# Optimization experiments

Hardware: AMD Instinct MI355X
Metric: run time of the kernel (lower is better)

## Reference

```python
import jax, jax.numpy as jnp
import numpy as np

B, S, D, F = 32, 512, 1024, 4096
R_COMMON, R_DOMAIN, E = 16, 16, 8
ALPHA = 2.0


def setup_inputs() -> dict:
    key = jax.random.key(0)
    ks = jax.random.split(key, 12)
    sd = lambda k, shape: jax.random.normal(k, shape, dtype=jnp.float32) * (1.0 / np.sqrt(shape[-1]))
    return {
        "hidden_states": jax.random.normal(ks[0], (B, S, D), dtype=jnp.float32),
        "expert_ids": jax.random.randint(ks[1], (B,), 0, E, dtype=jnp.int32),
        # nn.Linear weights: [out_features, in_features]
        "wi": sd(ks[2], (F, D)),
        "wo": sd(ks[3], (D, F)),
        "common_wi_a": sd(ks[4], (R_COMMON, D)),
        "common_wi_b": sd(ks[5], (F, R_COMMON)),
        "common_wo_a": sd(ks[6], (R_COMMON, F)),
        "common_wo_b": sd(ks[7], (D, R_COMMON)),
        # stacked per-expert LoRA weights
        "experts_wi_a": sd(ks[8], (E, R_DOMAIN, D)),
        "experts_wi_b": sd(ks[9], (F, R_DOMAIN)) * jnp.ones((E, 1, 1)) * 0.0 + sd(ks[9], (E, F, R_DOMAIN)),
        "experts_wo_a": sd(ks[10], (E, R_DOMAIN, F)),
        "experts_wo_b": sd(ks[11], (E, D, R_DOMAIN)),
    }


def _expert_lora(x, expert_ids, Wa, Wb):
    """Per-row (dim 0) expert LoRA correction, vectorized via gather.

    x: [B, S, din]; Wa: [E, r, din]; Wb: [E, dout, r].
    Equivalent to the per-expert mask-gather/scatter-add loop since each
    row belongs to exactly one expert.
    """
    Ab = Wa[expert_ids]  # [B, r, din]
    Bb = Wb[expert_ids]  # [B, dout, r]
    low = jnp.einsum("bsd,brd->bsr", x, Ab)
    return ALPHA * jnp.einsum("bsr,bor->bso", low, Bb)


def reference(hidden_states, expert_ids, wi, wo,
              common_wi_a, common_wi_b, common_wo_a, common_wo_b,
              experts_wi_a, experts_wi_b, experts_wo_a, experts_wo_b):
    x = hidden_states
    hidden_i = jnp.einsum("bsd,fd->bsf", x, wi)
    hidden_i += ALPHA * jnp.einsum("bsr,fr->bsf", jnp.einsum("bsd,rd->bsr", x, common_wi_a), common_wi_b)
    hidden_i += _expert_lora(x, expert_ids, experts_wi_a, experts_wi_b)
    hidden_i = jax.nn.relu(hidden_i)  # dense_act_fn='relu'; dropout is identity (eval)
    hidden_o = jnp.einsum("bsf,df->bsd", hidden_i, wo)
    hidden_o += ALPHA * jnp.einsum("bsr,dr->bsd", jnp.einsum("bsf,rf->bsr", hidden_i, common_wo_a), common_wo_b)
    hidden_o += _expert_lora(hidden_i, expert_ids, experts_wo_a, experts_wo_b)
    return hidden_o
```

## Files before the change

kernel.cpp:

```cpp
#include <hip/hip_runtime.h>
#include <hip/hip_bf16.h>
#include <stdint.h>

#define B_ 32
#define S_ 512
#define D_ 1024
#define F_ 4096
#define N_ (B_*S_)
#define E_ 8
#define ALPHA_ 2.0f

#define LDA1 1088
#define LDA2 4160

typedef __hip_bfloat16 bf16;
typedef __attribute__((ext_vector_type(8))) short short8;
typedef __attribute__((ext_vector_type(8))) __bf16 bf16x8;
typedef __attribute__((ext_vector_type(4))) float f32x4;

__device__ __forceinline__ f32x4 mfma_bf16(short8 a, short8 b, f32x4 c) {
    return __builtin_amdgcn_mfma_f32_16x16x32_bf16(
        __builtin_bit_cast(bf16x8, a), __builtin_bit_cast(bf16x8, b), c, 0, 0, 0);
}

__device__ __forceinline__ void gload_lds16(const void* g, void* l) {
    __builtin_amdgcn_global_load_lds((const __attribute__((address_space(1))) void*)g,
                                     (__attribute__((address_space(3))) void*)l, 16, 0, 0);
}

__device__ __forceinline__ unsigned pack2(float a, float b) {
    unsigned short x = __builtin_bit_cast(unsigned short, __float2bfloat16(a));
    unsigned short y = __builtin_bit_cast(unsigned short, __float2bfloat16(b));
    return (unsigned)x | ((unsigned)y << 16);
}
__device__ __forceinline__ uint2 pack4(float4 v) {
    return make_uint2(pack2(v.x, v.y), pack2(v.z, v.w));
}

__global__ __launch_bounds__(256) void prep_w_kernel(
    const float* __restrict__ wi, const float* __restrict__ wo,
    const float* __restrict__ cwia, const float* __restrict__ cwib,
    const float* __restrict__ cwoa, const float* __restrict__ cwob,
    const float* __restrict__ ewia, const float* __restrict__ ewib,
    const float* __restrict__ ewoa, const float* __restrict__ ewob,
    bf16* __restrict__ wi_b, bf16* __restrict__ wo_b,
    bf16* __restrict__ ex1, bf16* __restrict__ ex2,
    bf16* __restrict__ wilo, bf16* __restrict__ wolo)
{
    const int tid0 = blockIdx.x * blockDim.x + threadIdx.x;
    const int stride = gridDim.x * blockDim.x;

    for (int i = tid0; i < F_*D_/4; i += stride) {
        ((uint2*)wi_b)[i] = pack4(((const float4*)wi)[i]);
        ((uint2*)wo_b)[i] = pack4(((const float4*)wo)[i]);
    }
    for (int i = tid0; i < E_*F_*16; i += stride) {
        int e = i >> 16; int rem = i & 0xFFFF; int f = rem >> 4; int r = rem & 15;
        bf16* dst = ex1 + (((size_t)e*F_ + f) << 6);
        dst[r]      = __float2bfloat16(cwib[f*16 + r]);
        dst[16 + r] = __float2bfloat16(ewib[(((size_t)e*F_ + f) << 4) + r]);
        dst[32 + r] = __float2bfloat16(0.f);
        dst[48 + r] = __float2bfloat16(0.f);
    }
    for (int i = tid0; i < E_*D_*16; i += stride) {
        int e = i >> 14; int rem = i & 0x3FFF; int d = rem >> 4; int r = rem & 15;
        bf16* dst = ex2 + (((size_t)e*D_ + d) << 6);
        dst[r]      = __float2bfloat16(cwob[d*16 + r]);
        dst[16 + r] = __float2bfloat16(ewob[(((size_t)e*D_ + d) << 4) + r]);
        dst[32 + r] = __float2bfloat16(0.f);
        dst[48 + r] = __float2bfloat16(0.f);
    }
    for (int i = tid0; i < E_*32*(D_/4); i += stride) {
        int e = i / (32*(D_/4)); int rem = i - e*(32*(D_/4));
        int r = rem / (D_/4); int c4 = (rem % (D_/4)) * 4;
        const float* src = (r < 16) ? (cwia + (size_t)r*D_ + c4)
                                    : (ewia + ((size_t)(e*16 + (r-16)))*D_ + c4);
        *(uint2*)(wilo + ((size_t)(e*32 + r))*D_ + c4) = pack4(*(const float4*)src);
    }
    for (int i = tid0; i < E_*32*(F_/4); i += stride) {
        int e = i / (32*(F_/4)); int rem = i - e*(32*(F_/4));
        int r = rem / (F_/4); int c4 = (rem % (F_/4)) * 4;
        const float* src = (r < 16) ? (cwoa + (size_t)r*F_ + c4)
                                    : (ewoa + ((size_t)(e*16 + (r-16)))*F_ + c4);
        *(uint2*)(wolo + ((size_t)(e*32 + r))*F_ + c4) = pack4(*(const float4*)src);
    }
}

__global__ __launch_bounds__(256) void prep_x_kernel(
    const float* __restrict__ x, bf16* __restrict__ A1)
{
    const int tid0 = blockIdx.x * blockDim.x + threadIdx.x;
    const int stride = gridDim.x * blockDim.x;
    for (int i = tid0; i < N_*(D_/4); i += stride) {
        int row = i >> 8; int c4 = (i & 255) << 2;
        float4 v = *(const float4*)(x + (size_t)i * 4);
        *(uint2*)(A1 + (size_t)row*LDA1 + c4) = pack4(v);
    }
    for (int i = tid0; i < N_*8; i += stride) {
        int row = i >> 3; int c = (i & 7) << 2;
        *(uint2*)(A1 + (size_t)row*LDA1 + 1056 + c) = make_uint2(0u, 0u);
    }
}

template<int K>
__global__ __launch_bounds__(256) void lowproj_kernel(
    const bf16* __restrict__ A, const bf16* __restrict__ W,
    const int* __restrict__ eids, bf16* __restrict__ Out,
    int lda, int kout)
{
    constexpr int BM = 64, BK = 64;
    __shared__ __align__(16) bf16 Asm[BM*BK];
    __shared__ __align__(16) bf16 Wsm[32*BK];

    const int tid = threadIdx.x;
    const int row0 = blockIdx.x * BM;
    const int e = eids[row0 >> 9];
    const int w = tid >> 6, lane = tid & 63;
    const int tr = tid >> 3, ts = tid & 7;
    const int lrow = lane & 15;
    const int lk16 = (lane >> 4) << 4;

    f32x4 acc[2] = {};

    int aoff, woff[2];
    { int r = w*16 + lrow; aoff = r*128 + (lk16 ^ ((r & 7) << 4)); }
    #pragma unroll
    for (int n = 0; n < 2; ++n) {
        int r = n*16 + lrow; woff[n] = r*128 + (lk16 ^ ((r & 7) << 4));
    }
    const bf16* Wp = W + (size_t)e * 32 * K;

    #pragma unroll 1
    for (int kt = 0; kt < K/BK; ++kt) {
        const int k0 = kt * BK;
        #pragma unroll
        for (int i = 0; i < 2; ++i) {
            int row = tr + 32*i;
            int slot = ts ^ (row & 7);
            gload_lds16(A + (size_t)(row0 + row)*lda + k0 + slot*8,
                        (char*)Asm + row*128 + ts*16);
        }
        {
            int row = tr;
            int slot = ts ^ (row & 7);
            gload_lds16(Wp + (size_t)row*K + k0 + slot*8,
                        (char*)Wsm + row*128 + ts*16);
        }
        __syncthreads();
        #pragma unroll
        for (int kk = 0; kk < 2; ++kk) {
            short8 a = *(const short8*)((const char*)Asm + (aoff ^ (kk << 6)));
            #pragma unroll
            for (int n = 0; n < 2; ++n) {
                short8 b = *(const short8*)((const char*)Wsm + (woff[n] ^ (kk << 6)));
                acc[n] = mfma_bf16(a, b, acc[n]);
            }
        }
        __syncthreads();
    }

    const int jrow = (lane >> 4) << 2;
    #pragma unroll
    for (int n = 0; n < 2; ++n) {
        #pragma unroll
        for (int j = 0; j < 4; ++j) {
            int r = row0 + w*16 + jrow + j;
            int c = n*16 + lrow;
            Out[(size_t)r*lda + kout + c] = __float2bfloat16(ALPHA_ * acc[n][j]);
        }
    }
    #pragma unroll
    for (int i = 0; i < 8; ++i) {
        int idx = tid*8 + i;
        int r = idx >> 5, c = idx & 31;
        Out[(size_t)(row0 + r)*lda + kout + 32 + c] = __float2bfloat16(0.f);
    }
}

#define DSREAD(base, off) (*(const short8*)((const char*)(base) + (off)))
#define VMW4 asm volatile("s_waitcnt vmcnt(4)" ::: "memory")
#define VMW2 asm volatile("s_waitcnt vmcnt(2)" ::: "memory")
#define VMW0 asm volatile("s_waitcnt vmcnt(0)" ::: "memory")
#define VMNONE (void)0
#define BAR __builtin_amdgcn_s_barrier()

#define STAGE_A_HALF(KTN, AL, h)                                           \
  { const bf16* gpA_ = Ag + (size_t)(KTN)*64;                              \
    int rA_ = tr + 64*(h);                                                 \
    int sA_ = ts ^ (rA_ & 7);                                              \
    gload_lds16(gpA_ + (size_t)rA_*LDAe + sA_*8,                           \
                (char*)(AL) + rA_*128 + ts*16);                            \
    int rA2_ = rA_ + 128;                                                  \
    gload_lds16(gpA_ + (size_t)rA2_*LDAe + sA_*8,                          \
                (char*)(AL) + rA2_*128 + ts*16); }

#define STAGE_B_HALF(KTN, BL, h)                                           \
  { const bf16* gpB_; int bldB_; int bkB_;                                 \
    if ((KTN) < KMAIN_EL/64) { gpB_ = Bg; bldB_ = LDBe; bkB_ = (KTN)*64; } \
    else                     { gpB_ = Bxg; bldB_ = 64; bkB_ = 0; }         \
    int rB_ = (tr & 31) + 64*(tr >> 5) + 32*(h);                           \
    int sB_ = ts ^ (rB_ & 7);                                              \
    gload_lds16(gpB_ + (size_t)rB_*bldB_ + bkB_ + sB_*8,                   \
                (char*)(BL) + rB_*128 + ts*16);                            \
    int rB2_ = rB_ + 128;                                                  \
    gload_lds16(gpB_ + (size_t)rB2_*bldB_ + bkB_ + sB_*8,                  \
                (char*)(BL) + rB2_*128 + ts*16); }

#define RD_AF(dst, AC, base)                                               \
  _Pragma("unroll") for (int m_ = 0; m_ < 4; ++m_)                         \
    _Pragma("unroll") for (int k_ = 0; k_ < 2; ++k_)                       \
      dst[m_][k_] = DSREAD(AC, aoff[(base)+m_] ^ (k_ << 6));

#define RD_BQ(dst, BC, base)                                               \
  _Pragma("unroll") for (int n_ = 0; n_ < 2; ++n_)                         \
    _Pragma("unroll") for (int k_ = 0; k_ < 2; ++k_)                       \
      dst[n_][k_] = DSREAD(BC, boff[(base)+n_] ^ (k_ << 6));

#define MFMA16(afr, bqr, mb, nb)                                           \
  __builtin_amdgcn_s_setprio(1);                                           \
  _Pragma("unroll") for (int m_ = 0; m_ < 4; ++m_)                         \
    _Pragma("unroll") for (int n_ = 0; n_ < 2; ++n_)                       \
      _Pragma("unroll") for (int k_ = 0; k_ < 2; ++k_)                     \
        acc[(mb)+m_][(nb)+n_] =                                            \
            mfma_bf16(afr[m_][k_], bqr[n_][k_], acc[(mb)+m_][(nb)+n_]);    \
  __builtin_amdgcn_s_setprio(0);

#define TILE8(AC, BC, DOSTAGE, AN, BN, KTN, W1, W2, W4)                    \
  {                                                                        \
    short8 afl[4][2], afh[4][2], bql[2][2], bqh[2][2];                     \
                         \
    RD_AF(afl, AC, 0); RD_BQ(bql, BC, 0);                                  \
    if (DOSTAGE) { STAGE_A_HALF(KTN, AN, 0); }                             \
    W1; BAR;                                                               \
    MFMA16(afl, bql, 0, 0);                                                \
                                                                  \
    RD_BQ(bqh, BC, 2);                                                     \
    if (DOSTAGE) { STAGE_B_HALF(KTN, BN, 0); }                             \
    W2; BAR;                                                               \
    MFMA16(afl, bqh, 0, 2);                                                \
                                                              \
    RD_AF(afh, AC, 4);                                                     \
    if (DOSTAGE) { STAGE_B_HALF(KTN, BN, 1); }                             \
    MFMA16(afh, bql, 4, 0);                                                \
    if (DOSTAGE) { STAGE_A_HALF(KTN, AN, 1); }                             \
    W4; BAR;                                                               \
    MFMA16(afh, bqh, 4, 2);                                                \
  }

template<int KMAIN_EL, int LDAe, int LDBe, int LDCe, int NCOLSe, bool RELU_BF16>
__global__ __launch_bounds__(512, 2) void gemm256_kernel(
    const bf16* __restrict__ A, const bf16* __restrict__ Bmain,
    const bf16* __restrict__ Bextra, const int* __restrict__ eids,
    void* __restrict__ C)
{
    constexpr int MT = N_/256;
    constexpr int NT = NCOLSe/256;
    constexpr int NWG = MT*NT;
    constexpr int KTILES = KMAIN_EL/64 + 1;
    static_assert((KTILES & 1) == 1, "pair loop + tail assumes odd KTILES");
    static_assert(NWG % 8 == 0, "xcd swizzle needs nwg%8==0");
    constexpr int CPX = NWG/8;

    __shared__ __align__(16) bf16 As[2][256*64];
    __shared__ __align__(16) bf16 Bs[2][256*64];

    const int bid = blockIdx.x;
    const int wg = (bid & 7) * CPX + (bid >> 3);
    const int mt = wg % MT, nt = wg / MT;
    const int arow0 = mt * 256, bcol0 = nt * 256;
    const int e = eids[arow0 >> 9];

    const int tid = threadIdx.x;
    const int lane = tid & 63;
    const int wid = tid >> 6;
    const int wm = wid >> 2, wn = wid & 3;
    const int tr = tid >> 3, ts = tid & 7;

    const bf16* Ag  = A + (size_t)arow0 * LDAe;
    const bf16* Bg  = Bmain + (size_t)bcol0 * LDBe;
    const bf16* Bxg = Bextra + ((size_t)e * NCOLSe + bcol0) * 64;

    int aoff[8], boff[4];
    const int lk16 = (lane >> 4) << 4;
    #pragma unroll
    for (int m = 0; m < 8; ++m) {
        int r = wm*128 + m*16 + (lane & 15);
        aoff[m] = r*128 + (lk16 ^ ((r & 7) << 4));
    }
    #pragma unroll
    for (int n = 0; n < 4; ++n) {
        int r = wn*64 + n*16 + (lane & 15);
        boff[n] = r*128 + (lk16 ^ ((r & 7) << 4));
    }

    f32x4 acc[8][4] = {};

    STAGE_A_HALF(0, As[0], 0);
    STAGE_B_HALF(0, Bs[0], 0);
    STAGE_B_HALF(0, Bs[0], 1);
    STAGE_A_HALF(0, As[0], 1);
    VMW4; BAR;

    #pragma unroll 1
    for (int t = 0; t < KTILES - 1; t += 2) {
        TILE8(As[0], Bs[0], true, As[1], Bs[1], t + 1, VMW4, VMW4, VMW4);
        TILE8(As[1], Bs[1], true, As[0], Bs[0], t + 2, VMW4, VMW4, VMW4);
    }
    TILE8(As[0], Bs[0], false, As[1], Bs[1], 0, VMW2, VMW0, VMNONE);

    const int jrow = (lane >> 4) << 2;
    if constexpr (RELU_BF16) {
        bf16* Cb = (bf16*)C;
        #pragma unroll
        for (int m = 0; m < 8; ++m)
            #pragma unroll
            for (int j = 0; j < 4; ++j) {
                size_t rbase = (size_t)(arow0 + wm*128 + m*16 + jrow + j) * LDCe;
                #pragma unroll
                for (int n = 0; n < 4; ++n) {
                    float v = acc[m][n][j];
                    v = v > 0.f ? v : 0.f;
                    Cb[rbase + bcol0 + wn*64 + n*16 + (lane & 15)] = __float2bfloat16(v);
                }
            }
    } else {
        float* Cf = (float*)C;
        #pragma unroll
        for (int m = 0; m < 8; ++m)
            #pragma unroll
            for (int j = 0; j < 4; ++j) {
                size_t rbase = (size_t)(arow0 + wm*128 + m*16 + jrow + j) * LDCe;
                #pragma unroll
                for (int n = 0; n < 4; ++n)
                    Cf[rbase + bcol0 + wn*64 + n*16 + (lane & 15)] = acc[m][n][j];
            }
    }
}

extern "C" void kernel_launch(void* const* d_in, const int* in_sizes, int n_in,
                              void* d_out, int out_size, void* d_ws, size_t ws_size,
                              hipStream_t stream)
{
    const float* x    = (const float*)d_in[0];
    const int*   eids = (const int*)d_in[1];
    const float* wi   = (const float*)d_in[2];
    const float* wo   = (const float*)d_in[3];
    const float* cwia = (const float*)d_in[4];
    const float* cwib = (const float*)d_in[5];
    const float* cwoa = (const float*)d_in[6];
    const float* cwob = (const float*)d_in[7];
    const float* ewia = (const float*)d_in[8];
    const float* ewib = (const float*)d_in[9];
    const float* ewoa = (const float*)d_in[10];
    const float* ewob = (const float*)d_in[11];

    char* p = (char*)d_ws;
    bf16* A1   = (bf16*)p; p += (size_t)N_*LDA1*sizeof(bf16);
    bf16* A2   = (bf16*)p; p += (size_t)N_*LDA2*sizeof(bf16);
    bf16* wi_b = (bf16*)p; p += (size_t)F_*D_*sizeof(bf16);
    bf16* wo_b = (bf16*)p; p += (size_t)D_*F_*sizeof(bf16);
    bf16* ex1  = (bf16*)p; p += (size_t)E_*F_*64*sizeof(bf16);
    bf16* ex2  = (bf16*)p; p += (size_t)E_*D_*64*sizeof(bf16);
    bf16* wilo = (bf16*)p; p += (size_t)E_*32*D_*sizeof(bf16);
    bf16* wolo = (bf16*)p; p += (size_t)E_*32*F_*sizeof(bf16);

    prep_w_kernel<<<dim3(512), dim3(256), 0, stream>>>(
        wi, wo, cwia, cwib, cwoa, cwob, ewia, ewib, ewoa, ewob,
        wi_b, wo_b, ex1, ex2, wilo, wolo);

    prep_x_kernel<<<dim3(2048), dim3(256), 0, stream>>>(x, A1);

    lowproj_kernel<D_><<<dim3(N_/64), dim3(256), 0, stream>>>(
        A1, wilo, eids, A1, LDA1, D_);

    gemm256_kernel<D_, LDA1, D_, LDA2, F_, true>
        <<<dim3((N_/256)*(F_/256)), dim3(512), 0, stream>>>(A1, wi_b, ex1, eids, A2);

    lowproj_kernel<F_><<<dim3(N_/64), dim3(256), 0, stream>>>(
        A2, wolo, eids, A2, LDA2, F_);

    gemm256_kernel<F_, LDA2, F_, D_, D_, false>
        <<<dim3((N_/256)*(D_/256)), dim3(512), 0, stream>>>(A2, wo_b, ex2, eids, d_out);

    (void)in_sizes; (void)n_in; (void)out_size; (void)ws_size;
}
```

Before: 471.1 us.

## Fuse x conversion into low-rank projection and split low-rank activations into separate buffers

Removes the separate prep_x kernel by having the first low-rank projection kernel read fp32 x, convert it to bf16, write A1 and compute the LoRA low-rank activations in one pass. The low-rank activations now go to dedicated N×64 buffers instead of padded extra columns of A1/A2, so A1/A2 use unpadded strides and the GEMM's final K tile reads from the separate buffer. The low-rank kernel is rewritten to load fragments straight from global memory into registers, with no LDS staging or barriers. The risk is less coalesced direct global loads and power-of-two strides that may cause cache or channel conflicts.

```diff
diff --git a/kernel.cpp b/kernel.cpp
--- a/kernel.cpp
+++ b/kernel.cpp
@@ -10,13 +10,11 @@
 #define E_ 8
 #define ALPHA_ 2.0f
 
-#define LDA1 1088
-#define LDA2 4160
-
 typedef __hip_bfloat16 bf16;
 typedef __attribute__((ext_vector_type(8))) short short8;
 typedef __attribute__((ext_vector_type(8))) __bf16 bf16x8;
 typedef __attribute__((ext_vector_type(4))) float f32x4;
+typedef __attribute__((ext_vector_type(4))) unsigned int uint32x4;
 
 __device__ __forceinline__ f32x4 mfma_bf16(short8 a, short8 b, f32x4 c) {
     return __builtin_amdgcn_mfma_f32_16x16x32_bf16(
@@ -86,94 +84,54 @@
     }
 }
 
-__global__ __launch_bounds__(256) void prep_x_kernel(
-    const float* __restrict__ x, bf16* __restrict__ A1)
+template<int K, bool SRC_F32, bool WRITE_A>
+__global__ __launch_bounds__(256) void lowproj_reg_kernel(
+    const void* __restrict__ Asrc, const bf16* __restrict__ W,
+    const int* __restrict__ eids, bf16* __restrict__ lowX,
+    bf16* __restrict__ Aout)
 {
-    const int tid0 = blockIdx.x * blockDim.x + threadIdx.x;
-    const int stride = gridDim.x * blockDim.x;
-    for (int i = tid0; i < N_*(D_/4); i += stride) {
-        int row = i >> 8; int c4 = (i & 255) << 2;
-        float4 v = *(const float4*)(x + (size_t)i * 4);
-        *(uint2*)(A1 + (size_t)row*LDA1 + c4) = pack4(v);
-    }
-    for (int i = tid0; i < N_*8; i += stride) {
-        int row = i >> 3; int c = (i & 7) << 2;
-        *(uint2*)(A1 + (size_t)row*LDA1 + 1056 + c) = make_uint2(0u, 0u);
-    }
-}
-
-template<int K>
-__global__ __launch_bounds__(256) void lowproj_kernel(
-    const bf16* __restrict__ A, const bf16* __restrict__ W,
-    const int* __restrict__ eids, bf16* __restrict__ Out,
-    int lda, int kout)
-{
-    constexpr int BM = 64, BK = 64;
-    __shared__ __align__(16) bf16 Asm[BM*BK];
-    __shared__ __align__(16) bf16 Wsm[32*BK];
-
     const int tid = threadIdx.x;
-    const int row0 = blockIdx.x * BM;
-    const int e = eids[row0 >> 9];
-    const int w = tid >> 6, lane = tid & 63;
-    const int tr = tid >> 3, ts = tid & 7;
-    const int lrow = lane & 15;
-    const int lk16 = (lane >> 4) << 4;
-
-    f32x4 acc[2] = {};
-
-    int aoff, woff[2];
-    { int r = w*16 + lrow; aoff = r*128 + (lk16 ^ ((r & 7) << 4)); }
+    const int lane = tid & 63, w = tid >> 6;
+    const int row0 = blockIdx.x * 64 + w * 16;
+    const int e = eids[blockIdx.x >> 3];
+    const bf16* Wp = W + (size_t)e * 32 * K;
+    const int r = lane & 15, kq = lane >> 4;
+    const size_t arow = (size_t)(row0 + r) * K;
+    const size_t w0row = (size_t)r * K, w1row = (size_t)(r + 16) * K;
+
+    f32x4 acc0 = {}, acc1 = {};
+
+    #pragma unroll 4
+    for (int k0 = 0; k0 < K; k0 += 32) {
+        const int kk = k0 + kq * 8;
+        short8 a;
+        if constexpr (SRC_F32) {
+            const float* xs = (const float*)Asrc + arow + kk;
+            float4 v0 = *(const float4*)xs;
+            float4 v1 = *(const float4*)(xs + 4);
+            uint32x4 u;
+            u[0] = pack2(v0.x, v0.y); u[1] = pack2(v0.z, v0.w);
+            u[2] = pack2(v1.x, v1.y); u[3] = pack2(v1.z, v1.w);
+            a = __builtin_bit_cast(short8, u);
+            if constexpr (WRITE_A)
+                *(short8*)(Aout + arow + kk) = a;
+        } else {
+            a = *(const short8*)((const bf16*)Asrc + arow + kk);
+        }
+        short8 b0 = *(const short8*)(Wp + w0row + kk);
+        short8 b1 = *(const short8*)(Wp + w1row + kk);
+        acc0 = mfma_bf16(a, b0, acc0);
+        acc1 = mfma_bf16(a, b1, acc1);
+    }
+
+    const int orow = row0 + kq * 4;
     #pragma unroll
-    for (int n = 0; n < 2; ++n) {
-        int r = n*16 + lrow; woff[n] = r*128 + (lk16 ^ ((r & 7) << 4));
-    }
-    const bf16* Wp = W + (size_t)e * 32 * K;
-
-    #pragma unroll 1
-    for (int kt = 0; kt < K/BK; ++kt) {
-        const int k0 = kt * BK;
-        #pragma unroll
-        for (int i = 0; i < 2; ++i) {
-            int row = tr + 32*i;
-            int slot = ts ^ (row & 7);
-            gload_lds16(A + (size_t)(row0 + row)*lda + k0 + slot*8,
-                        (char*)Asm + row*128 + ts*16);
-        }
-        {
-            int row = tr;
-            int slot = ts ^ (row & 7);
-            gload_lds16(Wp + (size_t)row*K + k0 + slot*8,
-                        (char*)Wsm + row*128 + ts*16);
-        }
-        __syncthreads();
-        #pragma unroll
-        for (int kk = 0; kk < 2; ++kk) {
-            short8 a = *(const short8*)((const char*)Asm + (aoff ^ (kk << 6)));
-            #pragma unroll
-            for (int n = 0; n < 2; ++n) {
-                short8 b = *(const short8*)((const char*)Wsm + (woff[n] ^ (kk << 6)));
-                acc[n] = mfma_bf16(a, b, acc[n]);
-            }
-        }
-        __syncthreads();
-    }
-
-    const int jrow = (lane >> 4) << 2;
-    #pragma unroll
-    for (int n = 0; n < 2; ++n) {
-        #pragma unroll
-        for (int j = 0; j < 4; ++j) {
-            int r = row0 + w*16 + jrow + j;
-            int c = n*16 + lrow;
-            Out[(size_t)r*lda + kout + c] = __float2bfloat16(ALPHA_ * acc[n][j]);
-        }
-    }
-    #pragma unroll
-    for (int i = 0; i < 8; ++i) {
-        int idx = tid*8 + i;
-        int r = idx >> 5, c = idx & 31;
-        Out[(size_t)(row0 + r)*lda + kout + 32 + c] = __float2bfloat16(0.f);
+    for (int j = 0; j < 4; ++j) {
+        bf16* dst = lowX + (size_t)(orow + j) * 64;
+        dst[r]      = __float2bfloat16(ALPHA_ * acc0[j]);
+        dst[16 + r] = __float2bfloat16(ALPHA_ * acc1[j]);
+        dst[32 + r] = __float2bfloat16(0.f);
+        dst[48 + r] = __float2bfloat16(0.f);
     }
 }
 
@@ -185,13 +143,15 @@
 #define BAR __builtin_amdgcn_s_barrier()
 
 #define STAGE_A_HALF(KTN, AL, h)                                           \
-  { const bf16* gpA_ = Ag + (size_t)(KTN)*64;                              \
+  { const bf16* gpA_; int aldA_;                                           \
+    if ((KTN) < KMAIN_EL/64) { gpA_ = Ag + (size_t)(KTN)*64; aldA_ = LDAe; }\
+    else                     { gpA_ = Axg; aldA_ = 64; }                   \
     int rA_ = tr + 64*(h);                                                 \
-    int sA_ = ts ^ (rA_ & 7);                                              \
-    gload_lds16(gpA_ + (size_t)rA_*LDAe + sA_*8,                           \
+    int sA_ = ts ^ (rA_ & 7);                                               \
+    gload_lds16(gpA_ + (size_t)rA_*aldA_ + sA_*8,                          \
                 (char*)(AL) + rA_*128 + ts*16);                            \
     int rA2_ = rA_ + 128;                                                  \
-    gload_lds16(gpA_ + (size_t)rA2_*LDAe + sA_*8,                          \
+    gload_lds16(gpA_ + (size_t)rA2_*aldA_ + sA_*8,                         \
                 (char*)(AL) + rA2_*128 + ts*16); }
 
 #define STAGE_B_HALF(KTN, BL, h)                                           \
@@ -199,7 +159,7 @@
     if ((KTN) < KMAIN_EL/64) { gpB_ = Bg; bldB_ = LDBe; bkB_ = (KTN)*64; } \
     else                     { gpB_ = Bxg; bldB_ = 64; bkB_ = 0; }         \
     int rB_ = (tr & 31) + 64*(tr >> 5) + 32*(h);                           \
-    int sB_ = ts ^ (rB_ & 7);                                              \
+    int sB_ = ts ^ (rB_ & 7);                                               \
     gload_lds16(gpB_ + (size_t)rB_*bldB_ + bkB_ + sB_*8,                   \
                 (char*)(BL) + rB_*128 + ts*16);                            \
     int rB2_ = rB_ + 128;                                                  \
@@ -228,17 +188,14 @@
 #define TILE8(AC, BC, DOSTAGE, AN, BN, KTN, W1, W2, W4)                    \
   {                                                                        \
     short8 afl[4][2], afh[4][2], bql[2][2], bqh[2][2];                     \
-                         \
     RD_AF(afl, AC, 0); RD_BQ(bql, BC, 0);                                  \
     if (DOSTAGE) { STAGE_A_HALF(KTN, AN, 0); }                             \
     W1; BAR;                                                               \
     MFMA16(afl, bql, 0, 0);                                                \
-                                                                  \
     RD_BQ(bqh, BC, 2);                                                     \
     if (DOSTAGE) { STAGE_B_HALF(KTN, BN, 0); }                             \
     W2; BAR;                                                               \
     MFMA16(afl, bqh, 0, 2);                                                \
-                                                              \
     RD_AF(afh, AC, 4);                                                     \
     if (DOSTAGE) { STAGE_B_HALF(KTN, BN, 1); }                             \
     MFMA16(afh, bql, 4, 0);                                                \
@@ -250,8 +207,8 @@
 template<int KMAIN_EL, int LDAe, int LDBe, int LDCe, int NCOLSe, bool RELU_BF16>
 __global__ __launch_bounds__(512, 2) void gemm256_kernel(
     const bf16* __restrict__ A, const bf16* __restrict__ Bmain,
-    const bf16* __restrict__ Bextra, const int* __restrict__ eids,
-    void* __restrict__ C)
+    const bf16* __restrict__ Bextra, const bf16* __restrict__ Alow,
+    const int* __restrict__ eids, void* __restrict__ C)
 {
     constexpr int MT = N_/256;
     constexpr int NT = NCOLSe/256;
@@ -277,6 +234,7 @@
     const int tr = tid >> 3, ts = tid & 7;
 
     const bf16* Ag  = A + (size_t)arow0 * LDAe;
+    const bf16* Axg = Alow + (size_t)arow0 * 64;
     const bf16* Bg  = Bmain + (size_t)bcol0 * LDBe;
     const bf16* Bxg = Bextra + ((size_t)e * NCOLSe + bcol0) * 64;
 
@@ -355,8 +313,10 @@
     const float* ewob = (const float*)d_in[11];
 
     char* p = (char*)d_ws;
-    bf16* A1   = (bf16*)p; p += (size_t)N_*LDA1*sizeof(bf16);
-    bf16* A2   = (bf16*)p; p += (size_t)N_*LDA2*sizeof(bf16);
+    bf16* A1   = (bf16*)p; p += (size_t)N_*D_*sizeof(bf16);
+    bf16* A2   = (bf16*)p; p += (size_t)N_*F_*sizeof(bf16);
+    bf16* low1 = (bf16*)p; p += (size_t)N_*64*sizeof(bf16);
+    bf16* low2 = (bf16*)p; p += (size_t)N_*64*sizeof(bf16);
     bf16* wi_b = (bf16*)p; p += (size_t)F_*D_*sizeof(bf16);
     bf16* wo_b = (bf16*)p; p += (size_t)D_*F_*sizeof(bf16);
     bf16* ex1  = (bf16*)p; p += (size_t)E_*F_*64*sizeof(bf16);
@@ -368,19 +328,19 @@
         wi, wo, cwia, cwib, cwoa, cwob, ewia, ewib, ewoa, ewob,
         wi_b, wo_b, ex1, ex2, wilo, wolo);
 
-    prep_x_kernel<<<dim3(2048), dim3(256), 0, stream>>>(x, A1);
-
-    lowproj_kernel<D_><<<dim3(N_/64), dim3(256), 0, stream>>>(
-        A1, wilo, eids, A1, LDA1, D_);
-
-    gemm256_kernel<D_, LDA1, D_, LDA2, F_, true>
-        <<<dim3((N_/256)*(F_/256)), dim3(512), 0, stream>>>(A1, wi_b, ex1, eids, A2);
-
-    lowproj_kernel<F_><<<dim3(N_/64), dim3(256), 0, stream>>>(
-        A2, wolo, eids, A2, LDA2, F_);
-
-    gemm256_kernel<F_, LDA2, F_, D_, D_, false>
-        <<<dim3((N_/256)*(D_/256)), dim3(512), 0, stream>>>(A2, wo_b, ex2, eids, d_out);
+    lowproj_reg_kernel<D_, true, true><<<dim3(N_/64), dim3(256), 0, stream>>>(
+        x, wilo, eids, low1, A1);
+
+    gemm256_kernel<D_, D_, D_, F_, F_, true>
+        <<<dim3((N_/256)*(F_/256)), dim3(512), 0, stream>>>(
+        A1, wi_b, ex1, low1, eids, A2);
+
+    lowproj_reg_kernel<F_, false, false><<<dim3(N_/64), dim3(256), 0, stream>>>(
+        A2, wolo, eids, low2, nullptr);
+
+    gemm256_kernel<F_, F_, F_, D_, D_, false>
+        <<<dim3((N_/256)*(D_/256)), dim3(512), 0, stream>>>(
+        A2, wo_b, ex2, low2, eids, d_out);
 
     (void)in_sizes; (void)n_in; (void)out_size; (void)ws_size;
 }
```

New measurement: 483.8 us. 2.7% more time.
